# Optimization experiments

Hardware: AMD Instinct MI355X
Metric: run time of the kernel (lower is better)

The kernel has to match this reference:

```python
import jax, jax.numpy as jnp
import numpy as np

EPS = 1e-06
TOP_K = 2


def setup_inputs() -> dict:
    key = jax.random.key(0)
    k1, k2 = jax.random.split(key)
    B, S, H, E = 4, 4096, 2048, 64
    x = jax.random.normal(k1, (B, S, H), dtype=jnp.float32)
    per_dim_scale = jnp.ones((H,), dtype=jnp.float32)
    W = jax.random.normal(k2, (H, E), dtype=jnp.float32) * 0.02  # Dense kernel [H, E]
    return {"x": x, "per_dim_scale": per_dim_scale, "W": W}


def reference(x, per_dim_scale, W):
    H = x.shape[-1]
    x_flat = x.reshape(-1, H)  # [T, H]
    # Parameter-free RMSNorm (Gemma4VNorm)
    normed = x_flat * jax.lax.rsqrt(jnp.mean(jnp.square(x_flat), axis=-1, keepdims=True) + EPS)
    # scale by 1/sqrt(H), then learnable per-dim scale
    normed = normed * jnp.asarray(H, normed.dtype) ** -0.5
    normed = normed * per_dim_scale.astype(normed.dtype)
    router_logits = normed @ W  # [T, E]
    router_probs = jax.nn.softmax(router_logits.astype(jnp.float32), axis=-1).astype(x.dtype)
    top_k_probs, top_k_indices = jax.lax.top_k(router_probs, TOP_K)  # [T, k]
    denom = jnp.maximum(jnp.sum(top_k_probs, axis=-1, keepdims=True),
                        jnp.asarray(1e-09, top_k_probs.dtype))
    top_k_probs = top_k_probs / denom
    # Sparse dispatch weights [T, E] (sum of scaled one-hots == scatter-add)
    T = router_probs.shape[0]
    rows = jnp.arange(T)[:, None]  # [T, 1] broadcast against [T, k]
    dispatch_weights = jnp.zeros_like(router_probs).at[rows, top_k_indices].add(top_k_probs)
    return dispatch_weights
```

## Files before the change

kernel.cpp:

```cpp
#include <hip/hip_runtime.h>
#include <math.h>

#define H 2048
#define E 64
#define TAU 1e-6f

#define MT 16
#define KCW 16

#define RB 16
#define CB 512
#define NCH (H / CB)
#define PITCH 516

#define WHI_OFF 65792u
#define WFRAG_BYTES 262144u
#define WLO_OFF (WHI_OFF + WFRAG_BYTES)
#define WS_NEEDED ((size_t)(WLO_OFF + WFRAG_BYTES))

typedef __attribute__((ext_vector_type(8))) short short8;
typedef __attribute__((ext_vector_type(4))) float f32x4;

__device__ __forceinline__ unsigned short bf16_rne(float f) {
    unsigned u = __float_as_uint(f);
    unsigned r = u + 0x7fffu + ((u >> 16) & 1u);
    return (unsigned short)(r >> 16);
}

__global__ __launch_bounds__(64)
void prep_w(const float* __restrict__ Wm, const float* __restrict__ pds,
            int* __restrict__ flags,
            unsigned short* __restrict__ whi, unsigned short* __restrict__ wlo)
{
    const int fb   = blockIdx.x;
    const int lane = threadIdx.x;
    if (fb == 0 && lane == 0) flags[0] = 0;
    const int kc  = fb >> 2;
    const int n   = fb & 3;
    const int r0  = kc * 32 + (lane >> 4) * 8;
    const int col = n * 16 + (lane & 15);

    short8 hv, lv;
#pragma unroll
    for (int j = 0; j < 8; ++j) {
        const int r = r0 + j;
        const double w = (double)pds[r] * (double)Wm[r * E + col];
        const unsigned short hb = bf16_rne((float)w);
        const double hd = (double)__uint_as_float((unsigned)hb << 16);
        const unsigned short lb = bf16_rne((float)(w - hd));
        hv[j] = (short)hb;
        lv[j] = (short)lb;
    }
    const size_t off = ((size_t)fb * 64 + lane) * 8;
    *(short8*)(whi + off) = hv;
    *(short8*)(wlo + off) = lv;
}

__global__ __launch_bounds__(256, 1)
void router_df(const float* __restrict__ x,
               const unsigned short* __restrict__ whi,
               const unsigned short* __restrict__ wlo,
               float* __restrict__ out,
               int* __restrict__ flags)
{
    __shared__ float lbuf[4][MT * E];
    __shared__ float ssbuf[64];
    __shared__ float sfac[16];

    const int t    = threadIdx.x;
    const int wid  = t >> 6;
    const int lane = t & 63;
    const int lsub = lane & 15;
    const int lgrp = lane >> 4;
    const int row0 = blockIdx.x * MT;

    const float* xbase = x + (size_t)(row0 + lsub) * H + wid * 512 + lgrp * 8;

    f32x4 acc[4] = {{0.f,0.f,0.f,0.f},{0.f,0.f,0.f,0.f},
                    {0.f,0.f,0.f,0.f},{0.f,0.f,0.f,0.f}};
    float sq = 0.0f;

    for (int kl = 0; kl < KCW; ++kl) {
        const float4 a0 = *(const float4*)(xbase + kl * 32);
        const float4 a1 = *(const float4*)(xbase + kl * 32 + 4);

        const int kc = wid * KCW + kl;
        const unsigned short* ph = whi + ((size_t)kc * 256 + lane) * 8;
        const unsigned short* pl = wlo + ((size_t)kc * 256 + lane) * 8;
        short8 bh[4], bl[4];
#pragma unroll
        for (int n = 0; n < 4; ++n) {
            bh[n] = *(const short8*)(ph + n * 512);
            bl[n] = *(const short8*)(pl + n * 512);
        }

        sq += a0.x * a0.x + a0.y * a0.y + a0.z * a0.z + a0.w * a0.w
            + a1.x * a1.x + a1.y * a1.y + a1.z * a1.z + a1.w * a1.w;

        const float xf[8] = { a0.x, a0.y, a0.z, a0.w, a1.x, a1.y, a1.z, a1.w };
        short8 ah, al;
#pragma unroll
        for (int e = 0; e < 8; ++e) {
            const unsigned short hb = bf16_rne(xf[e]);
            const unsigned short lb = bf16_rne(xf[e] - __uint_as_float((unsigned)hb << 16));
            ah[e] = (short)hb;
            al[e] = (short)lb;
        }

#pragma unroll
        for (int n = 0; n < 4; ++n) {
            acc[n] = __builtin_amdgcn_mfma_f32_16x16x32_bf16(ah, bh[n], acc[n], 0, 0, 0);
            acc[n] = __builtin_amdgcn_mfma_f32_16x16x32_bf16(ah, bl[n], acc[n], 0, 0, 0);
            acc[n] = __builtin_amdgcn_mfma_f32_16x16x32_bf16(al, bh[n], acc[n], 0, 0, 0);
        }
    }

#pragma unroll
    for (int n = 0; n < 4; ++n)
#pragma unroll
        for (int q = 0; q < 4; ++q)
            lbuf[wid][(lgrp * 4 + q) * E + n * 16 + lsub] = acc[n][q];

    sq += __shfl_xor(sq, 16);
    sq += __shfl_xor(sq, 32);
    if (lane < 16) ssbuf[wid * 16 + lane] = sq;
    __syncthreads();

    if (t < 16) {
        const float tot = ssbuf[t] + ssbuf[16 + t] + ssbuf[32 + t] + ssbuf[48 + t];
        sfac[t] = rsqrtf(tot * (1.0f / (float)H) + 1e-6f) * 0.022097086912079608f;
    }
    __syncthreads();

#pragma unroll
    for (int rr = 0; rr < 4; ++rr) {
        const int r = wid * 4 + rr;
        const float L = (lbuf[0][r * E + lane] + lbuf[1][r * E + lane]
                       + lbuf[2][r * E + lane] + lbuf[3][r * E + lane]) * sfac[r];

        float m = L;
#pragma unroll
        for (int off = 32; off >= 1; off >>= 1)
            m = fmaxf(m, __shfl_xor(m, off));
        const float ev = expf(L - m);
        float S = ev;
#pragma unroll
        for (int off = 32; off >= 1; off >>= 1)
            S += __shfl_xor(S, off);
        const float p = ev / S;

        float v1 = p; int i1 = lane;
#pragma unroll
        for (int off = 32; off >= 1; off >>= 1) {
            const float ov = __shfl_xor(v1, off);
            const int   oi = __shfl_xor(i1, off);
            if (ov > v1 || (ov == v1 && oi < i1)) { v1 = ov; i1 = oi; }
        }
        float v2 = (lane == i1) ? -1.0f : p; int i2 = lane;
#pragma unroll
        for (int off = 32; off >= 1; off >>= 1) {
            const float ov = __shfl_xor(v2, off);
            const int   oi = __shfl_xor(i2, off);
            if (ov > v2 || (ov == v2 && oi < i2)) { v2 = ov; i2 = oi; }
        }
        float v3 = (lane == i1 || lane == i2) ? -1.0f : p;
#pragma unroll
        for (int off = 32; off >= 1; off >>= 1)
            v3 = fmaxf(v3, __shfl_xor(v3, off));

        if (lane == 0 && (v2 - v3) < TAU) {
            const int k = atomicAdd(flags, 1);
            flags[1 + k] = row0 + r;
        }

        const float denom = fmaxf(v1 + v2, 1e-9f);
        const float wA = v1 / denom;
        const float wB = v2 / denom;
        const float o  = (lane == i1) ? wA : ((lane == i2) ? wB : 0.0f);
        out[(size_t)(row0 + r) * E + lane] = o;
    }
}

__global__ __launch_bounds__(256)
void router_fix(const float* __restrict__ x,
                const float* __restrict__ pds,
                const float* __restrict__ Wm,
                float* __restrict__ out,
                const int* __restrict__ flags)
{
    __shared__ double yd[H];
    __shared__ double parts[4 * E];
    __shared__ double ss[256];

    const int t = threadIdx.x;
    const int count = flags[0];

    for (int j = blockIdx.x; j < count; j += gridDim.x) {
        const int r = flags[1 + j];
        const float* xr = x + (size_t)r * H;

        double s = 0.0;
#pragma unroll
        for (int i = 0; i < 8; ++i) {
            const int h = t * 8 + i;
            const double xv = (double)xr[h];
            s += xv * xv;
            yd[h] = xv * (double)pds[h];
        }
        ss[t] = s;
        __syncthreads();

        const int ex = t & 63;
        const int sl = t >> 6;
        const float* wp = Wm + (size_t)(sl * 512) * E + ex;
        double acc = 0.0;
#pragma unroll 8
        for (int h = 0; h < 512; ++h)
            acc = fma(yd[sl * 512 + h], (double)wp[(size_t)h * E], acc);
        parts[sl * E + ex] = acc;
        __syncthreads();

        if (t < 64) {
            const int lane = t;
            double tot = ss[lane * 4] + ss[lane * 4 + 1] + ss[lane * 4 + 2] + ss[lane * 4 + 3];
#pragma unroll
            for (int off = 32; off >= 1; off >>= 1)
                tot += __shfl_xor(tot, off);
            const double sf = (1.0 / sqrt(tot * (1.0 / (double)H) + 1e-6)) * 0.022097086912079608;

            const double Ld = parts[0 * E + lane] + parts[1 * E + lane]
                            + parts[2 * E + lane] + parts[3 * E + lane];
            const float L = (float)(Ld * sf);

            float m = L;
#pragma unroll
            for (int off = 32; off >= 1; off >>= 1)
                m = fmaxf(m, __shfl_xor(m, off));
            const float ev = (float)exp((double)(L - m));
            float S = ev;
#pragma unroll
            for (int off = 32; off >= 1; off >>= 1)
                S += __shfl_xor(S, off);
            const float p = ev / S;

            float v1 = p; int i1 = lane;
#pragma unroll
            for (int off = 32; off >= 1; off >>= 1) {
                const float ov = __shfl_xor(v1, off);
                const int   oi = __shfl_xor(i1, off);
                if (ov > v1 || (ov == v1 && oi < i1)) { v1 = ov; i1 = oi; }
            }
            float v2 = (lane == i1) ? -1.0f : p; int i2 = lane;
#pragma unroll
            for (int off = 32; off >= 1; off >>= 1) {
                const float ov = __shfl_xor(v2, off);
                const int   oi = __shfl_xor(i2, off);
                if (ov > v2 || (ov == v2 && oi < i2)) { v2 = ov; i2 = oi; }
            }

            const float denom = fmaxf(v1 + v2, 1e-9f);
            const float wA = v1 / denom;
            const float wB = v2 / denom;
            const float o  = (lane == i1) ? wA : ((lane == i2) ? wB : 0.0f);
            out[(size_t)r * E + lane] = o;
        }
        __syncthreads();
    }
}

__global__ void zero_cnt(int* __restrict__ flags) {
    if (threadIdx.x == 0 && blockIdx.x == 0) flags[0] = 0;
}

__global__ __launch_bounds__(256)
void router_f32(const float* __restrict__ x,
                const float* __restrict__ pds,
                const float* __restrict__ Wm,
                float* __restrict__ out,
                int* __restrict__ flags)
{
    __shared__ __align__(16) float yb[RB * PITCH];
    __shared__ float ssbuf[256];
    __shared__ float sfac[RB];

    const int t    = threadIdx.x;
    const int wv_i = t >> 6;
    const int lane = t & 63;
    const int g    = lane >> 4;
    const int e0   = (lane & 15) << 2;

    const int row0 = blockIdx.x * RB;
    const int srow = t >> 4;
    const int sseg = t & 15;

    const float* xrow = x + (size_t)(row0 + srow) * H;

    float acc[4][4];
#pragma unroll
    for (int a = 0; a < 4; ++a)
#pragma unroll
        for (int b = 0; b < 4; ++b) acc[a][b] = 0.0f;

    float sumsq = 0.0f;
    float4 xv[8];
#pragma unroll
    for (int i = 0; i < 8; ++i)
        xv[i] = *(const float4*)(xrow + sseg * 4 + i * 64);

    for (int c = 0; c < NCH; ++c) {
        const float* pbase = pds + c * CB;
#pragma unroll
        for (int i = 0; i < 8; ++i) {
            const int hl = sseg * 4 + i * 64;
            const float4 a4 = xv[i];
            const float4 p4 = *(const float4*)(pbase + hl);
            sumsq += a4.x * a4.x + a4.y * a4.y + a4.z * a4.z + a4.w * a4.w;
            float4 y4;
            y4.x = a4.x * p4.x; y4.y = a4.y * p4.y;
            y4.z = a4.z * p4.z; y4.w = a4.w * p4.w;
            *(float4*)(&yb[srow * PITCH + hl]) = y4;
        }
        __syncthreads();

        if (c + 1 < NCH) {
            const int h0n = (c + 1) * CB;
#pragma unroll
            for (int i = 0; i < 8; ++i)
                xv[i] = *(const float4*)(xrow + h0n + sseg * 4 + i * 64);
        }

        const int hb = wv_i * 128;
        const float* wbase = Wm + (size_t)(c * CB) * E + e0;
#pragma unroll 2
        for (int s = 0; s < 32; ++s) {
            const int hh = hb + s * 4;
            const float4 w0 = *(const float4*)(wbase + (size_t)(hh + 0) * E);
            const float4 w1 = *(const float4*)(wbase + (size_t)(hh + 1) * E);
            const float4 w2 = *(const float4*)(wbase + (size_t)(hh + 2) * E);
            const float4 w3 = *(const float4*)(wbase + (size_t)(hh + 3) * E);
#pragma unroll
            for (int rr = 0; rr < 4; ++rr) {
                const float4 y4 = *(const float4*)(&yb[(4 * rr + g) * PITCH + hh]);
                acc[rr][0] = fmaf(y4.w, w3.x, fmaf(y4.z, w2.x, fmaf(y4.y, w1.x, fmaf(y4.x, w0.x, acc[rr][0]))));
                acc[rr][1] = fmaf(y4.w, w3.y, fmaf(y4.z, w2.y, fmaf(y4.y, w1.y, fmaf(y4.x, w0.y, acc[rr][1]))));
                acc[rr][2] = fmaf(y4.w, w3.z, fmaf(y4.z, w2.z, fmaf(y4.y, w1.z, fmaf(y4.x, w0.z, acc[rr][2]))));
                acc[rr][3] = fmaf(y4.w, w3.w, fmaf(y4.z, w2.w, fmaf(y4.y, w1.w, fmaf(y4.x, w0.w, acc[rr][3]))));
            }
        }
        __syncthreads();
    }

    ssbuf[t] = sumsq;
    __syncthreads();
    if (t < RB) {
        float tot = 0.0f;
#pragma unroll
        for (int i = 0; i < 16; ++i) tot += ssbuf[t * 16 + i];
        sfac[t] = rsqrtf(tot * (1.0f / (float)H) + 1e-6f) * 0.022097086912079608f;
    }

#pragma unroll
    for (int rr = 0; rr < 4; ++rr) {
        const int r = 4 * rr + g;
        *(float4*)(&yb[((wv_i * RB) + r) * E + e0]) =
            make_float4(acc[rr][0], acc[rr][1], acc[rr][2], acc[rr][3]);
    }
    __syncthreads();

#pragma unroll
    for (int rr = 0; rr < 4; ++rr) {
        const int r = wv_i * 4 + rr;
        float L = yb[(0 * RB + r) * E + lane] + yb[(1 * RB + r) * E + lane]
                + yb[(2 * RB + r) * E + lane] + yb[(3 * RB + r) * E + lane];
        L *= sfac[r];

        float m = L;
#pragma unroll
        for (int off = 32; off >= 1; off >>= 1)
            m = fmaxf(m, __shfl_xor(m, off));
        const float ev = expf(L - m);
        float S = ev;
#pragma unroll
        for (int off = 32; off >= 1; off >>= 1)
            S += __shfl_xor(S, off);
        const float p = ev / S;

        float v1 = p; int i1 = lane;
#pragma unroll
        for (int off = 32; off >= 1; off >>= 1) {
            const float ov = __shfl_xor(v1, off);
            const int   oi = __shfl_xor(i1, off);
            if (ov > v1 || (ov == v1 && oi < i1)) { v1 = ov; i1 = oi; }
        }
        float v2 = (lane == i1) ? -1.0f : p; int i2 = lane;
#pragma unroll
        for (int off = 32; off >= 1; off >>= 1) {
            const float ov = __shfl_xor(v2, off);
            const int   oi = __shfl_xor(i2, off);
            if (ov > v2 || (ov == v2 && oi < i2)) { v2 = ov; i2 = oi; }
        }
        float v3 = (lane == i1 || lane == i2) ? -1.0f : p;
#pragma unroll
        for (int off = 32; off >= 1; off >>= 1)
            v3 = fmaxf(v3, __shfl_xor(v3, off));

        if (lane == 0 && (v2 - v3) < TAU) {
            const int k = atomicAdd(flags, 1);
            flags[1 + k] = row0 + r;
        }

        const float denom = fmaxf(v1 + v2, 1e-9f);
        const float wA = v1 / denom;
        const float wB = v2 / denom;
        const float o  = (lane == i1) ? wA : ((lane == i2) ? wB : 0.0f);
        out[(size_t)(row0 + r) * E + lane] = o;
    }
}

extern "C" void kernel_launch(void* const* d_in, const int* in_sizes, int n_in,
                              void* d_out, int out_size, void* d_ws, size_t ws_size,
                              hipStream_t stream) {
    const float* x   = (const float*)d_in[0];
    const float* pds = (const float*)d_in[1];
    const float* Wm  = (const float*)d_in[2];
    float* out = (float*)d_out;
    int* flags = (int*)d_ws;

    const int T = in_sizes[0] / H;

    if (ws_size >= WS_NEEDED) {
        unsigned short* whi = (unsigned short*)((char*)d_ws + WHI_OFF);
        unsigned short* wlo = (unsigned short*)((char*)d_ws + WLO_OFF);
        hipLaunchKernelGGL(prep_w,     dim3(256),    dim3(64),  0, stream, Wm, pds, flags, whi, wlo);
        hipLaunchKernelGGL(router_df,  dim3(T / MT), dim3(256), 0, stream, x, whi, wlo, out, flags);
        hipLaunchKernelGGL(router_fix, dim3(128),    dim3(256), 0, stream, x, pds, Wm, out, flags);
    } else {
        hipLaunchKernelGGL(zero_cnt,   dim3(1),      dim3(64),  0, stream, flags);
        hipLaunchKernelGGL(router_f32, dim3(T / RB), dim3(256), 0, stream, x, pds, Wm, out, flags);
        hipLaunchKernelGGL(router_fix, dim3(128),    dim3(256), 0, stream, x, pds, Wm, out, flags);
    }
}
```

Before: 87.52 us.

## Stream x through LDS with async global_load_lds double buffering

Replaces direct per-lane float4 loads of x in the router GEMM with direct global-to-LDS copies (global_load_lds) into a swizzled, double-buffered per-wave LDS region, prefetching the next 128-column stage while the current one is consumed by MFMA. W fragments are batched four k-chunks at a time into registers, and launch bounds are raised to two blocks per CU. The aim is better memory-level parallelism and latency hiding on the bandwidth-bound x stream. The cost is 32 KB of LDS per block plus a large register footprint (32 short8 W fragments), which may cap occupancy or cause spills.

```diff
diff --git a/kernel.cpp b/kernel.cpp
--- a/kernel.cpp
+++ b/kernel.cpp
@@ -6,7 +6,7 @@
 #define TAU 1e-6f
 
 #define MT 16
-#define KCW 16
+#define NST 4
 
 #define RB 16
 #define CB 512
@@ -25,6 +25,13 @@
     unsigned u = __float_as_uint(f);
     unsigned r = u + 0x7fffu + ((u >> 16) & 1u);
     return (unsigned short)(r >> 16);
+}
+
+__device__ __forceinline__ void glds16(const float* src, float* dst) {
+    __builtin_amdgcn_global_load_lds(
+        (const __attribute__((address_space(1))) unsigned int*)src,
+        (__attribute__((address_space(3))) unsigned int*)dst,
+        16, 0, 0);
 }
 
 __global__ __launch_bounds__(64)
@@ -56,14 +63,14 @@
     *(short8*)(wlo + off) = lv;
 }
 
-__global__ __launch_bounds__(256, 1)
-void router_df(const float* __restrict__ x,
-               const unsigned short* __restrict__ whi,
-               const unsigned short* __restrict__ wlo,
-               float* __restrict__ out,
-               int* __restrict__ flags)
+__global__ __launch_bounds__(256, 2)
+void router_glds(const float* __restrict__ x,
+                 const unsigned short* __restrict__ whi,
+                 const unsigned short* __restrict__ wlo,
+                 float* __restrict__ out,
+                 int* __restrict__ flags)
 {
-    __shared__ float lbuf[4][MT * E];
+    __shared__ __align__(16) float smem[4 * 2 * 2048];
     __shared__ float ssbuf[64];
     __shared__ float sfac[16];
 
@@ -74,52 +81,99 @@
     const int lgrp = lane >> 4;
     const int row0 = blockIdx.x * MT;
 
-    const float* xbase = x + (size_t)(row0 + lsub) * H + wid * 512 + lgrp * 8;
+    const float* xq = x + (size_t)row0 * H + wid * 512;
+
+    int soff[8];
+#pragma unroll
+    for (int i = 0; i < 8; ++i) {
+        const int g = i * 64 + lane;
+        const int r = g >> 5;
+        const int u = g & 31;
+        const int sw = (r & 7) ^ ((r & 3) << 3);
+        soff[i] = r * H + ((u ^ sw) << 2);
+    }
+    const int swr = (lsub & 7) ^ ((lsub & 3) << 3);
+    float* mybuf = &smem[wid * 4096];
 
     f32x4 acc[4] = {{0.f,0.f,0.f,0.f},{0.f,0.f,0.f,0.f},
                     {0.f,0.f,0.f,0.f},{0.f,0.f,0.f,0.f}};
     float sq = 0.0f;
 
-    for (int kl = 0; kl < KCW; ++kl) {
-        const float4 a0 = *(const float4*)(xbase + kl * 32);
-        const float4 a1 = *(const float4*)(xbase + kl * 32 + 4);
-
-        const int kc = wid * KCW + kl;
-        const unsigned short* ph = whi + ((size_t)kc * 256 + lane) * 8;
-        const unsigned short* pl = wlo + ((size_t)kc * 256 + lane) * 8;
-        short8 bh[4], bl[4];
-#pragma unroll
-        for (int n = 0; n < 4; ++n) {
-            bh[n] = *(const short8*)(ph + n * 512);
-            bl[n] = *(const short8*)(pl + n * 512);
-        }
-
-        sq += a0.x * a0.x + a0.y * a0.y + a0.z * a0.z + a0.w * a0.w
-            + a1.x * a1.x + a1.y * a1.y + a1.z * a1.z + a1.w * a1.w;
-
-        const float xf[8] = { a0.x, a0.y, a0.z, a0.w, a1.x, a1.y, a1.z, a1.w };
-        short8 ah, al;
-#pragma unroll
-        for (int e = 0; e < 8; ++e) {
-            const unsigned short hb = bf16_rne(xf[e]);
-            const unsigned short lb = bf16_rne(xf[e] - __uint_as_float((unsigned)hb << 16));
-            ah[e] = (short)hb;
-            al[e] = (short)lb;
-        }
-
-#pragma unroll
-        for (int n = 0; n < 4; ++n) {
-            acc[n] = __builtin_amdgcn_mfma_f32_16x16x32_bf16(ah, bh[n], acc[n], 0, 0, 0);
-            acc[n] = __builtin_amdgcn_mfma_f32_16x16x32_bf16(ah, bl[n], acc[n], 0, 0, 0);
-            acc[n] = __builtin_amdgcn_mfma_f32_16x16x32_bf16(al, bh[n], acc[n], 0, 0, 0);
-        }
-    }
+#pragma unroll
+    for (int i = 0; i < 8; ++i)
+        glds16(xq + soff[i], mybuf + i * 256);
+
+    for (int st = 0; st < NST; ++st) {
+        const int b = st & 1;
+        float* cur = mybuf + b * 2048;
+
+        asm volatile("s_waitcnt vmcnt(0)" ::: "memory");
+
+        short8 WH[16], WL[16];
+#pragma unroll
+        for (int kl = 0; kl < 4; ++kl) {
+            const size_t kc = (size_t)(wid * 16 + st * 4 + kl);
+            const unsigned short* ph = whi + (kc * 256 + lane) * 8;
+            const unsigned short* pl = wlo + (kc * 256 + lane) * 8;
+#pragma unroll
+            for (int n = 0; n < 4; ++n) {
+                WH[kl * 4 + n] = *(const short8*)(ph + n * 512);
+                WL[kl * 4 + n] = *(const short8*)(pl + n * 512);
+            }
+        }
+        __builtin_amdgcn_sched_barrier(0);
+
+        float4 xa[4], xb[4];
+        const float* rbase = cur + lsub * 128;
+#pragma unroll
+        for (int kl = 0; kl < 4; ++kl) {
+            const int v0 = kl * 8 + lgrp * 2;
+            xa[kl] = *(const float4*)(rbase + ((v0 ^ swr) << 2));
+            xb[kl] = *(const float4*)(rbase + (((v0 + 1) ^ swr) << 2));
+        }
+        __builtin_amdgcn_sched_barrier(0);
+
+        if (st + 1 < NST) {
+            float* nxt = mybuf + (b ^ 1) * 2048;
+            const float* xs = xq + (st + 1) * 128;
+#pragma unroll
+            for (int i = 0; i < 8; ++i)
+                glds16(xs + soff[i], nxt + i * 256);
+        }
+        __builtin_amdgcn_sched_barrier(0);
+
+#pragma unroll
+        for (int kl = 0; kl < 4; ++kl) {
+            const float4 a0 = xa[kl];
+            const float4 a1 = xb[kl];
+            sq += a0.x * a0.x + a0.y * a0.y + a0.z * a0.z + a0.w * a0.w
+                + a1.x * a1.x + a1.y * a1.y + a1.z * a1.z + a1.w * a1.w;
+            const float xf[8] = { a0.x, a0.y, a0.z, a0.w, a1.x, a1.y, a1.z, a1.w };
+            short8 ah, al;
+#pragma unroll
+            for (int e = 0; e < 8; ++e) {
+                const unsigned short hb = bf16_rne(xf[e]);
+                const unsigned short lb = bf16_rne(xf[e] - __uint_as_float((unsigned)hb << 16));
+                ah[e] = (short)hb;
+                al[e] = (short)lb;
+            }
+#pragma unroll
+            for (int n = 0; n < 4; ++n) {
+                acc[n] = __builtin_amdgcn_mfma_f32_16x16x32_bf16(ah, WH[kl * 4 + n], acc[n], 0, 0, 0);
+                acc[n] = __builtin_amdgcn_mfma_f32_16x16x32_bf16(ah, WL[kl * 4 + n], acc[n], 0, 0, 0);
+                acc[n] = __builtin_amdgcn_mfma_f32_16x16x32_bf16(al, WH[kl * 4 + n], acc[n], 0, 0, 0);
+            }
+        }
+    }
+
+    __syncthreads();
+    float* lbuf = smem;
 
 #pragma unroll
     for (int n = 0; n < 4; ++n)
 #pragma unroll
         for (int q = 0; q < 4; ++q)
-            lbuf[wid][(lgrp * 4 + q) * E + n * 16 + lsub] = acc[n][q];
+            lbuf[wid * 1024 + (lgrp * 4 + q) * E + n * 16 + lsub] = acc[n][q];
 
     sq += __shfl_xor(sq, 16);
     sq += __shfl_xor(sq, 32);
@@ -135,8 +189,8 @@
 #pragma unroll
     for (int rr = 0; rr < 4; ++rr) {
         const int r = wid * 4 + rr;
-        const float L = (lbuf[0][r * E + lane] + lbuf[1][r * E + lane]
-                       + lbuf[2][r * E + lane] + lbuf[3][r * E + lane]) * sfac[r];
+        const float L = (lbuf[r * E + lane]        + lbuf[1024 + r * E + lane]
+                       + lbuf[2048 + r * E + lane] + lbuf[3072 + r * E + lane]) * sfac[r];
 
         float m = L;
 #pragma unroll
@@ -431,12 +485,12 @@
     if (ws_size >= WS_NEEDED) {
         unsigned short* whi = (unsigned short*)((char*)d_ws + WHI_OFF);
         unsigned short* wlo = (unsigned short*)((char*)d_ws + WLO_OFF);
-        hipLaunchKernelGGL(prep_w,     dim3(256),    dim3(64),  0, stream, Wm, pds, flags, whi, wlo);
-        hipLaunchKernelGGL(router_df,  dim3(T / MT), dim3(256), 0, stream, x, whi, wlo, out, flags);
-        hipLaunchKernelGGL(router_fix, dim3(128),    dim3(256), 0, stream, x, pds, Wm, out, flags);
+        hipLaunchKernelGGL(prep_w,      dim3(256),    dim3(64),  0, stream, Wm, pds, flags, whi, wlo);
+        hipLaunchKernelGGL(router_glds, dim3(T / MT), dim3(256), 0, stream, x, whi, wlo, out, flags);
+        hipLaunchKernelGGL(router_fix,  dim3(128),    dim3(256), 0, stream, x, pds, Wm, out, flags);
     } else {
-        hipLaunchKernelGGL(zero_cnt,   dim3(1),      dim3(64),  0, stream, flags);
-        hipLaunchKernelGGL(router_f32, dim3(T / RB), dim3(256), 0, stream, x, pds, Wm, out, flags);
-        hipLaunchKernelGGL(router_fix, dim3(128),    dim3(256), 0, stream, x, pds, Wm, out, flags);
-    }
-}
+        hipLaunchKernelGGL(zero_cnt,    dim3(1),      dim3(64),  0, stream, flags);
+        hipLaunchKernelGGL(router_f32,  dim3(T / RB), dim3(256), 0, stream, x, pds, Wm, out, flags);
+        hipLaunchKernelGGL(router_fix,  dim3(128),    dim3(256), 0, stream, x, pds, Wm, out, flags);
+    }
+}
```

After: 92.08 us. 5.2% more time.

## Stage x tiles through swizzled LDS with coalesced loads and batched W prefetch

Applied to the files above, without the earlier changes.

Replaces per-lane strided x loads (each lane reading its own row) with fully coalesced block-wide float4 row loads. Each element is split once into bf16 hi/lo and written to XOR-swizzled shared memory, which waves then read back as MFMA A fragments. W fragments are loaded in batches of 16 before the MFMAs, with sched barriers to keep the loads grouped. Launch bounds are raised to 2 blocks per CU to improve latency hiding. The cost is extra LDS traffic, two block-wide syncs per half, and recomputing the sum of squares from the hi+lo reconstruction, which is slightly less exact.

```diff
diff --git a/kernel.cpp b/kernel.cpp
--- a/kernel.cpp
+++ b/kernel.cpp
@@ -6,7 +6,6 @@
 #define TAU 1e-6f
 
 #define MT 16
-#define KCW 16
 
 #define RB 16
 #define CB 512
@@ -56,14 +55,14 @@
     *(short8*)(wlo + off) = lv;
 }
 
-__global__ __launch_bounds__(256, 1)
-void router_df(const float* __restrict__ x,
+__global__ __launch_bounds__(256, 2)
+void router_ct(const float* __restrict__ x,
                const unsigned short* __restrict__ whi,
                const unsigned short* __restrict__ wlo,
                float* __restrict__ out,
                int* __restrict__ flags)
 {
-    __shared__ float lbuf[4][MT * E];
+    __shared__ __align__(16) unsigned short xb[2][MT][1024];
     __shared__ float ssbuf[64];
     __shared__ float sfac[16];
 
@@ -74,52 +73,94 @@
     const int lgrp = lane >> 4;
     const int row0 = blockIdx.x * MT;
 
-    const float* xbase = x + (size_t)(row0 + lsub) * H + wid * 512 + lgrp * 8;
+    const int wunit = t >> 1;
+    const int wsub  = (t & 1) * 4;
 
     f32x4 acc[4] = {{0.f,0.f,0.f,0.f},{0.f,0.f,0.f,0.f},
                     {0.f,0.f,0.f,0.f},{0.f,0.f,0.f,0.f}};
     float sq = 0.0f;
 
-    for (int kl = 0; kl < KCW; ++kl) {
-        const float4 a0 = *(const float4*)(xbase + kl * 32);
-        const float4 a1 = *(const float4*)(xbase + kl * 32 + 4);
-
-        const int kc = wid * KCW + kl;
-        const unsigned short* ph = whi + ((size_t)kc * 256 + lane) * 8;
-        const unsigned short* pl = wlo + ((size_t)kc * 256 + lane) * 8;
-        short8 bh[4], bl[4];
-#pragma unroll
-        for (int n = 0; n < 4; ++n) {
-            bh[n] = *(const short8*)(ph + n * 512);
-            bl[n] = *(const short8*)(pl + n * 512);
-        }
-
-        sq += a0.x * a0.x + a0.y * a0.y + a0.z * a0.z + a0.w * a0.w
-            + a1.x * a1.x + a1.y * a1.y + a1.z * a1.z + a1.w * a1.w;
-
-        const float xf[8] = { a0.x, a0.y, a0.z, a0.w, a1.x, a1.y, a1.z, a1.w };
-        short8 ah, al;
-#pragma unroll
-        for (int e = 0; e < 8; ++e) {
-            const unsigned short hb = bf16_rne(xf[e]);
-            const unsigned short lb = bf16_rne(xf[e] - __uint_as_float((unsigned)hb << 16));
-            ah[e] = (short)hb;
-            al[e] = (short)lb;
-        }
-
-#pragma unroll
-        for (int n = 0; n < 4; ++n) {
-            acc[n] = __builtin_amdgcn_mfma_f32_16x16x32_bf16(ah, bh[n], acc[n], 0, 0, 0);
-            acc[n] = __builtin_amdgcn_mfma_f32_16x16x32_bf16(ah, bl[n], acc[n], 0, 0, 0);
-            acc[n] = __builtin_amdgcn_mfma_f32_16x16x32_bf16(al, bh[n], acc[n], 0, 0, 0);
-        }
-    }
-
+#pragma unroll
+    for (int h = 0; h < 2; ++h) {
+#pragma unroll
+        for (int b2 = 0; b2 < 2; ++b2) {
+            float4 xv[8];
+#pragma unroll
+            for (int j = 0; j < 8; ++j) {
+                const int i = b2 * 8 + j;
+                xv[j] = *(const float4*)(x + (size_t)(row0 + i) * H + h * 1024 + t * 4);
+            }
+#pragma unroll
+            for (int j = 0; j < 8; ++j) {
+                const int i = b2 * 8 + j;
+                const float f[4] = { xv[j].x, xv[j].y, xv[j].z, xv[j].w };
+                unsigned hu[4], lu[4];
+#pragma unroll
+                for (int e = 0; e < 4; ++e) {
+                    const unsigned short hb = bf16_rne(f[e]);
+                    const unsigned short lb = bf16_rne(f[e] - __uint_as_float((unsigned)hb << 16));
+                    hu[e] = hb; lu[e] = lb;
+                }
+                const int uph = wunit ^ (i & 7);
+                const int idx = uph * 8 + wsub;
+                *(uint2*)(&xb[0][i][idx]) = make_uint2(hu[0] | (hu[1] << 16), hu[2] | (hu[3] << 16));
+                *(uint2*)(&xb[1][i][idx]) = make_uint2(lu[0] | (lu[1] << 16), lu[2] | (lu[3] << 16));
+            }
+        }
+        __syncthreads();
+
+#pragma unroll
+        for (int g = 0; g < 2; ++g) {
+            short8 WH[16], WL[16];
+#pragma unroll
+            for (int kl = 0; kl < 4; ++kl) {
+                const size_t kc = (size_t)(h * 32 + wid * 8 + g * 4 + kl);
+                const unsigned short* ph = whi + (kc * 256 + lane) * 8;
+                const unsigned short* pl = wlo + (kc * 256 + lane) * 8;
+#pragma unroll
+                for (int n = 0; n < 4; ++n) {
+                    WH[kl * 4 + n] = *(const short8*)(ph + n * 512);
+                    WL[kl * 4 + n] = *(const short8*)(pl + n * 512);
+                }
+            }
+            __builtin_amdgcn_sched_barrier(0);
+
+            short8 AH[4], AL[4];
+#pragma unroll
+            for (int kl = 0; kl < 4; ++kl) {
+                const int v   = wid * 32 + (g * 4 + kl) * 4 + lgrp;
+                const int idx = lsub * 1024 + (v ^ (lsub & 7)) * 8;
+                AH[kl] = *(const short8*)(&xb[0][0][idx]);
+                AL[kl] = *(const short8*)(&xb[1][0][idx]);
+            }
+            __builtin_amdgcn_sched_barrier(0);
+
+#pragma unroll
+            for (int kl = 0; kl < 4; ++kl) {
+#pragma unroll
+                for (int e = 0; e < 8; ++e) {
+                    const float hf = __uint_as_float(((unsigned)(unsigned short)AH[kl][e]) << 16);
+                    const float lf = __uint_as_float(((unsigned)(unsigned short)AL[kl][e]) << 16);
+                    const float xr = hf + lf;
+                    sq = fmaf(xr, xr, sq);
+                }
+#pragma unroll
+                for (int n = 0; n < 4; ++n) {
+                    acc[n] = __builtin_amdgcn_mfma_f32_16x16x32_bf16(AH[kl], WH[kl * 4 + n], acc[n], 0, 0, 0);
+                    acc[n] = __builtin_amdgcn_mfma_f32_16x16x32_bf16(AH[kl], WL[kl * 4 + n], acc[n], 0, 0, 0);
+                    acc[n] = __builtin_amdgcn_mfma_f32_16x16x32_bf16(AL[kl], WH[kl * 4 + n], acc[n], 0, 0, 0);
+                }
+            }
+        }
+        __syncthreads();
+    }
+
+    float* lbuf = (float*)xb;
 #pragma unroll
     for (int n = 0; n < 4; ++n)
 #pragma unroll
         for (int q = 0; q < 4; ++q)
-            lbuf[wid][(lgrp * 4 + q) * E + n * 16 + lsub] = acc[n][q];
+            lbuf[wid * 1024 + (lgrp * 4 + q) * E + n * 16 + lsub] = acc[n][q];
 
     sq += __shfl_xor(sq, 16);
     sq += __shfl_xor(sq, 32);
@@ -135,8 +176,8 @@
 #pragma unroll
     for (int rr = 0; rr < 4; ++rr) {
         const int r = wid * 4 + rr;
-        const float L = (lbuf[0][r * E + lane] + lbuf[1][r * E + lane]
-                       + lbuf[2][r * E + lane] + lbuf[3][r * E + lane]) * sfac[r];
+        const float L = (lbuf[r * E + lane]        + lbuf[1024 + r * E + lane]
+                       + lbuf[2048 + r * E + lane] + lbuf[3072 + r * E + lane]) * sfac[r];
 
         float m = L;
 #pragma unroll
@@ -432,7 +473,7 @@
         unsigned short* whi = (unsigned short*)((char*)d_ws + WHI_OFF);
         unsigned short* wlo = (unsigned short*)((char*)d_ws + WLO_OFF);
         hipLaunchKernelGGL(prep_w,     dim3(256),    dim3(64),  0, stream, Wm, pds, flags, whi, wlo);
-        hipLaunchKernelGGL(router_df,  dim3(T / MT), dim3(256), 0, stream, x, whi, wlo, out, flags);
+        hipLaunchKernelGGL(router_ct,  dim3(T / MT), dim3(256), 0, stream, x, whi, wlo, out, flags);
         hipLaunchKernelGGL(router_fix, dim3(128),    dim3(256), 0, stream, x, pds, Wm, out, flags);
     } else {
         hipLaunchKernelGGL(zero_cnt,   dim3(1),      dim3(64),  0, stream, flags);
```

After: 94.70 us. +8.2%, slower.

## Widen router tile to 64 rows with 8 waves reusing W fragments

Applied to the files above, without the earlier changes.

The main router kernel now handles 64 token rows per block with 512 threads (8 waves). Each wave covers 256 columns of H and reuses each loaded W hi/lo fragment across four 16-row tiles. Partial logits from the two halves of the waves are combined in shared memory over two synchronised passes. This cuts W fragment traffic per row and gives more MFMA work per load. In exchange it uses many more accumulator registers (64 floats of acc), shared memory grows to 64KB of lbuf, and there are 4x fewer blocks (256), which may limit occupancy.

```diff
diff --git a/kernel.cpp b/kernel.cpp
--- a/kernel.cpp
+++ b/kernel.cpp
@@ -5,8 +5,7 @@
 #define E 64
 #define TAU 1e-6f
 
-#define MT 16
-#define KCW 16
+#define MT 64
 
 #define RB 16
 #define CB 512
@@ -56,16 +55,16 @@
     *(short8*)(wlo + off) = lv;
 }
 
-__global__ __launch_bounds__(256, 1)
-void router_df(const float* __restrict__ x,
+__global__ __launch_bounds__(512, 2)
+void router_4t(const float* __restrict__ x,
                const unsigned short* __restrict__ whi,
                const unsigned short* __restrict__ wlo,
                float* __restrict__ out,
                int* __restrict__ flags)
 {
     __shared__ float lbuf[4][MT * E];
-    __shared__ float ssbuf[64];
-    __shared__ float sfac[16];
+    __shared__ float ssbuf[8][MT];
+    __shared__ float sfac[MT];
 
     const int t    = threadIdx.x;
     const int wid  = t >> 6;
@@ -74,67 +73,100 @@
     const int lgrp = lane >> 4;
     const int row0 = blockIdx.x * MT;
 
-    const float* xbase = x + (size_t)(row0 + lsub) * H + wid * 512 + lgrp * 8;
-
-    f32x4 acc[4] = {{0.f,0.f,0.f,0.f},{0.f,0.f,0.f,0.f},
-                    {0.f,0.f,0.f,0.f},{0.f,0.f,0.f,0.f}};
-    float sq = 0.0f;
-
-    for (int kl = 0; kl < KCW; ++kl) {
-        const float4 a0 = *(const float4*)(xbase + kl * 32);
-        const float4 a1 = *(const float4*)(xbase + kl * 32 + 4);
-
-        const int kc = wid * KCW + kl;
+    f32x4 acc[4][4];
+#pragma unroll
+    for (int a = 0; a < 4; ++a)
+#pragma unroll
+        for (int b = 0; b < 4; ++b) acc[a][b] = (f32x4){0.f, 0.f, 0.f, 0.f};
+    float sq[4] = {0.f, 0.f, 0.f, 0.f};
+
+    const float* xw = x + (size_t)row0 * H + wid * 256 + lgrp * 8;
+
+    for (int kl = 0; kl < 8; ++kl) {
+        const int kc = wid * 8 + kl;
+
         const unsigned short* ph = whi + ((size_t)kc * 256 + lane) * 8;
         const unsigned short* pl = wlo + ((size_t)kc * 256 + lane) * 8;
-        short8 bh[4], bl[4];
+        short8 WH[4], WL[4];
 #pragma unroll
         for (int n = 0; n < 4; ++n) {
-            bh[n] = *(const short8*)(ph + n * 512);
-            bl[n] = *(const short8*)(pl + n * 512);
-        }
-
-        sq += a0.x * a0.x + a0.y * a0.y + a0.z * a0.z + a0.w * a0.w
-            + a1.x * a1.x + a1.y * a1.y + a1.z * a1.z + a1.w * a1.w;
-
-        const float xf[8] = { a0.x, a0.y, a0.z, a0.w, a1.x, a1.y, a1.z, a1.w };
-        short8 ah, al;
-#pragma unroll
-        for (int e = 0; e < 8; ++e) {
-            const unsigned short hb = bf16_rne(xf[e]);
-            const unsigned short lb = bf16_rne(xf[e] - __uint_as_float((unsigned)hb << 16));
-            ah[e] = (short)hb;
-            al[e] = (short)lb;
-        }
-
-#pragma unroll
-        for (int n = 0; n < 4; ++n) {
-            acc[n] = __builtin_amdgcn_mfma_f32_16x16x32_bf16(ah, bh[n], acc[n], 0, 0, 0);
-            acc[n] = __builtin_amdgcn_mfma_f32_16x16x32_bf16(ah, bl[n], acc[n], 0, 0, 0);
-            acc[n] = __builtin_amdgcn_mfma_f32_16x16x32_bf16(al, bh[n], acc[n], 0, 0, 0);
-        }
-    }
-
-#pragma unroll
-    for (int n = 0; n < 4; ++n)
-#pragma unroll
-        for (int q = 0; q < 4; ++q)
-            lbuf[wid][(lgrp * 4 + q) * E + n * 16 + lsub] = acc[n][q];
-
-    sq += __shfl_xor(sq, 16);
-    sq += __shfl_xor(sq, 32);
-    if (lane < 16) ssbuf[wid * 16 + lane] = sq;
+            WH[n] = *(const short8*)(ph + n * 512);
+            WL[n] = *(const short8*)(pl + n * 512);
+        }
+
+        float4 a0[4], a1[4];
+#pragma unroll
+        for (int tt = 0; tt < 4; ++tt) {
+            const float* p = xw + (size_t)(tt * 16 + lsub) * H + kl * 32;
+            a0[tt] = *(const float4*)p;
+            a1[tt] = *(const float4*)(p + 4);
+        }
+
+        short8 AH[4], AL[4];
+#pragma unroll
+        for (int tt = 0; tt < 4; ++tt) {
+            const float f[8] = { a0[tt].x, a0[tt].y, a0[tt].z, a0[tt].w,
+                                 a1[tt].x, a1[tt].y, a1[tt].z, a1[tt].w };
+            sq[tt] += f[0]*f[0] + f[1]*f[1] + f[2]*f[2] + f[3]*f[3]
+                    + f[4]*f[4] + f[5]*f[5] + f[6]*f[6] + f[7]*f[7];
+#pragma unroll
+            for (int e = 0; e < 8; ++e) {
+                const unsigned short hb = bf16_rne(f[e]);
+                const unsigned short lb = bf16_rne(f[e] - __uint_as_float((unsigned)hb << 16));
+                AH[tt][e] = (short)hb;
+                AL[tt][e] = (short)lb;
+            }
+        }
+
+#pragma unroll
+        for (int tt = 0; tt < 4; ++tt)
+#pragma unroll
+            for (int n = 0; n < 4; ++n) {
+                acc[tt][n] = __builtin_amdgcn_mfma_f32_16x16x32_bf16(AH[tt], WH[n], acc[tt][n], 0, 0, 0);
+                acc[tt][n] = __builtin_amdgcn_mfma_f32_16x16x32_bf16(AH[tt], WL[n], acc[tt][n], 0, 0, 0);
+                acc[tt][n] = __builtin_amdgcn_mfma_f32_16x16x32_bf16(AL[tt], WH[n], acc[tt][n], 0, 0, 0);
+            }
+    }
+
+#pragma unroll
+    for (int tt = 0; tt < 4; ++tt) {
+        float s = sq[tt];
+        s += __shfl_xor(s, 16);
+        s += __shfl_xor(s, 32);
+        if (lane < 16) ssbuf[wid][tt * 16 + lane] = s;
+    }
+
+    if (wid < 4) {
+#pragma unroll
+        for (int tt = 0; tt < 4; ++tt)
+#pragma unroll
+            for (int n = 0; n < 4; ++n)
+#pragma unroll
+                for (int q = 0; q < 4; ++q)
+                    lbuf[wid][(tt * 16 + lgrp * 4 + q) * E + n * 16 + lsub] = acc[tt][n][q];
+    }
     __syncthreads();
-
-    if (t < 16) {
-        const float tot = ssbuf[t] + ssbuf[16 + t] + ssbuf[32 + t] + ssbuf[48 + t];
+    if (wid >= 4) {
+#pragma unroll
+        for (int tt = 0; tt < 4; ++tt)
+#pragma unroll
+            for (int n = 0; n < 4; ++n)
+#pragma unroll
+                for (int q = 0; q < 4; ++q)
+                    lbuf[wid - 4][(tt * 16 + lgrp * 4 + q) * E + n * 16 + lsub] += acc[tt][n][q];
+    }
+    __syncthreads();
+
+    if (t < MT) {
+        const float tot = ssbuf[0][t] + ssbuf[1][t] + ssbuf[2][t] + ssbuf[3][t]
+                        + ssbuf[4][t] + ssbuf[5][t] + ssbuf[6][t] + ssbuf[7][t];
         sfac[t] = rsqrtf(tot * (1.0f / (float)H) + 1e-6f) * 0.022097086912079608f;
     }
     __syncthreads();
 
 #pragma unroll
-    for (int rr = 0; rr < 4; ++rr) {
-        const int r = wid * 4 + rr;
+    for (int rr = 0; rr < 8; ++rr) {
+        const int r = wid * 8 + rr;
         const float L = (lbuf[0][r * E + lane] + lbuf[1][r * E + lane]
                        + lbuf[2][r * E + lane] + lbuf[3][r * E + lane]) * sfac[r];
 
@@ -432,7 +464,7 @@
         unsigned short* whi = (unsigned short*)((char*)d_ws + WHI_OFF);
         unsigned short* wlo = (unsigned short*)((char*)d_ws + WLO_OFF);
         hipLaunchKernelGGL(prep_w,     dim3(256),    dim3(64),  0, stream, Wm, pds, flags, whi, wlo);
-        hipLaunchKernelGGL(router_df,  dim3(T / MT), dim3(256), 0, stream, x, whi, wlo, out, flags);
+        hipLaunchKernelGGL(router_4t,  dim3(T / MT), dim3(512), 0, stream, x, whi, wlo, out, flags);
         hipLaunchKernelGGL(router_fix, dim3(128),    dim3(256), 0, stream, x, pds, Wm, out, flags);
     } else {
         hipLaunchKernelGGL(zero_cnt,   dim3(1),      dim3(64),  0, stream, flags);
```

New measurement: 83.30 us (median of 2 runs). 1.05x faster.
